# Optimization experiments

Measured on AMD Instinct MI355X. Metric: run time of the kernel, lower is better.

Reference implementation:

```python
import jax, jax.numpy as jnp
import numpy as np

B, S, E, H = 2, 2048, 1024, 16
DH = E // H


def setup_inputs() -> dict:
    key = jax.random.key(0)
    ks = jax.random.split(key, 9)
    s = 1.0 / np.sqrt(E)
    return {
        "queries": jax.random.normal(ks[0], (B, S, E), dtype=jnp.float32),
        "keys": jax.random.normal(ks[1], (B, S, E), dtype=jnp.float32),
        "values": jax.random.normal(ks[2], (B, S, E), dtype=jnp.float32),
        "mask": jax.random.randint(ks[3], (B, 1, 1, S), 0, 2, dtype=jnp.int32),
        "Wq": jax.random.normal(ks[4], (E, E), dtype=jnp.float32) * s,
        "Wk": jax.random.normal(ks[5], (E, E), dtype=jnp.float32) * s,
        "Wv": jax.random.normal(ks[6], (E, E), dtype=jnp.float32) * s,
        "Wo": jax.random.normal(ks[7], (E, E), dtype=jnp.float32) * s,
        "bo": jax.random.normal(ks[8], (E,), dtype=jnp.float32) * s,
    }


def reference(queries, keys, values, mask, Wq, Wk, Wv, Wo, bo):
    n, d_q, _ = queries.shape
    d_k = keys.shape[1]
    # Linear projections (torch Linear: x @ W.T), then split into heads
    q = (queries @ Wq.T).reshape(n, d_q, H, DH)
    k = (keys @ Wk.T).reshape(n, d_k, H, DH)
    v = (values @ Wv.T).reshape(n, d_k, H, DH)
    # [n, H, d_q, d_k] attention scores
    energy = jnp.einsum("nqhd,nkhd->nhqk", q, k)
    energy = jnp.where(mask == 0, jnp.float32(-1e20), energy)
    # NOTE: original scales by sqrt(key seq length), not head dim -- kept faithful
    attn = jax.nn.softmax(energy / jnp.sqrt(jnp.float32(d_k)), axis=3)
    out = jnp.einsum("nhql,nlhd->nqhd", attn, v).reshape(n, d_q, E)
    return out @ Wo.T + bo
```

## Files before the change

### kernel.cpp

```cpp
#include <hip/hip_runtime.h>
#include <hip/hip_bf16.h>

#define BB 2
#define SS 2048
#define EE 1024
#define HH 16
#define DHH 64

using bf16x8 = __attribute__((ext_vector_type(8))) __bf16;
using f32x4  = __attribute__((ext_vector_type(4))) float;

#if __has_builtin(__builtin_amdgcn_exp2f)
#define EXP2(x) __builtin_amdgcn_exp2f(x)
#else
#define EXP2(x) __exp2f(x)
#endif

static __device__ __forceinline__ unsigned short f2bf(float f) {
    unsigned int u = __float_as_uint(f);
    u += 0x7FFFu + ((u >> 16) & 1u);
    return (unsigned short)(u >> 16);
}

static __device__ __forceinline__ unsigned int pk2bf(float lo, float hi) {
    union { __hip_bfloat162 h2; unsigned int u; } c;
    c.h2 = __float22bfloat162_rn(float2{lo, hi});
    return c.u;
}

static __device__ __forceinline__ void async_load16(const void* g, void* l) {
    __builtin_amdgcn_global_load_lds(
        (const __attribute__((address_space(1))) unsigned int*)g,
        (__attribute__((address_space(3))) unsigned int*)l, 16, 0, 0);
}

__global__ void cvt_kernel(const float* __restrict__ W0, const float* __restrict__ W1,
                           const float* __restrict__ W2, const float* __restrict__ W3,
                           const float* __restrict__ X0, const float* __restrict__ X1,
                           const float* __restrict__ X2,
                           unsigned short* __restrict__ Wb,
                           unsigned short* __restrict__ D0, unsigned short* __restrict__ D1,
                           unsigned short* __restrict__ D2)
{
    const int z = blockIdx.y;
    const float* src;
    unsigned short* dst;
    if (z < 4) {
        if (blockIdx.x >= 512) return;
        src = (z == 0) ? W0 : (z == 1) ? W1 : (z == 2) ? W2 : W3;
        dst = Wb + (size_t)z * 1048576;
    } else {
        src = (z == 4) ? X0 : (z == 5) ? X1 : X2;
        dst = (z == 4) ? D0 : (z == 5) ? D1 : D2;
    }
    const size_t base = (size_t)blockIdx.x * 2048 + (size_t)threadIdx.x * 8;
    const float4 f0 = *(const float4*)(src + base);
    const float4 f1 = *(const float4*)(src + base + 4);
    uint4 p;
    p.x = pk2bf(f0.x, f0.y); p.y = pk2bf(f0.z, f0.w);
    p.z = pk2bf(f1.x, f1.y); p.w = pk2bf(f1.z, f1.w);
    *(uint4*)(dst + base) = p;
}

template<int MT, int NT, bool BF16OUT, bool VT_Z2>
__global__ __launch_bounds__(256, 3)
void gemm_xwt(const unsigned short* __restrict__ X0, const unsigned short* __restrict__ X1,
              const unsigned short* __restrict__ X2,
              const unsigned short* __restrict__ W0, const unsigned short* __restrict__ W1,
              const unsigned short* __restrict__ W2,
              void* __restrict__ Y0, void* __restrict__ Y1, void* __restrict__ Y2,
              const float* __restrict__ bias, int M, int N, int K,
              float s0, float s1, float s2)
{
    constexpr int BK = 32;
    constexpr int NI = MT / 32;
    constexpr int NJ = NT / 32;
    __shared__ __align__(16) unsigned short As[2][MT * BK];
    __shared__ __align__(16) unsigned short Bs[2][NT * BK];

    const int z = blockIdx.z;
    const unsigned short* __restrict__ X = (z == 0) ? X0 : ((z == 1) ? X1 : X2);
    const unsigned short* __restrict__ W = (z == 0) ? W0 : ((z == 1) ? W1 : W2);
    void* __restrict__ Y                 = (z == 0) ? Y0 : ((z == 1) ? Y1 : Y2);
    const float ysc                      = (z == 0) ? s0 : ((z == 1) ? s1 : s2);

    const int tid  = threadIdx.x;
    const int lane = tid & 63;
    const int wave = tid >> 6;
    const int wm   = (wave >> 1) * (MT / 2);
    const int wn   = (wave & 1) * (NT / 2);
    const int m0   = blockIdx.y * MT;
    const int n0   = blockIdx.x * NT;
    const int l16  = lane & 15;
    const int quad = lane >> 4;

    const int arow = lane >> 2;
    const int akc  = (lane & 3) * 8;

    f32x4 acc[NI][NJ];
    #pragma unroll
    for (int i = 0; i < NI; i++)
        #pragma unroll
        for (int j = 0; j < NJ; j++) acc[i][j] = f32x4{0.f, 0.f, 0.f, 0.f};

    auto stage = [&](int k0, int buf) {
        #pragma unroll
        for (int j = 0; j < NT / 64; j++) {
            const int rr = wave * (NT / 4) + j * 16;
            async_load16(W + (size_t)(n0 + rr + arow) * K + k0 + akc, Bs[buf] + rr * BK);
        }
        #pragma unroll
        for (int j = 0; j < MT / 64; j++) {
            const int rr = wave * (MT / 4) + j * 16;
            async_load16(X + (size_t)(m0 + rr + arow) * K + k0 + akc, As[buf] + rr * BK);
        }
    };

    stage(0, 0);
    const int niter = K / BK;
    for (int i = 0; i < niter; i++) {
        const int cur = i & 1;
        __syncthreads();
        if (i + 1 < niter) stage((i + 1) * BK, cur ^ 1);

        bf16x8 afrag[NI], bfrag[NJ];
        #pragma unroll
        for (int ii = 0; ii < NI; ii++)
            afrag[ii] = *(const bf16x8*)(As[cur] + (wm + ii * 16 + l16) * BK + quad * 8);
        #pragma unroll
        for (int j = 0; j < NJ; j++)
            bfrag[j] = *(const bf16x8*)(Bs[cur] + (wn + j * 16 + l16) * BK + quad * 8);
        #pragma unroll
        for (int ii = 0; ii < NI; ii++)
            #pragma unroll
            for (int j = 0; j < NJ; j++)
                acc[ii][j] = __builtin_amdgcn_mfma_f32_16x16x32_bf16(afrag[ii], bfrag[j], acc[ii][j], 0, 0, 0);
    }

    if (BF16OUT && VT_Z2 && z == 2) {
        #pragma unroll
        for (int i = 0; i < NI; i++) {
            const int row0 = m0 + wm + i * 16 + quad * 4;
            const int bb   = row0 >> 11;
            const int sx   = row0 & (SS - 1);
            #pragma unroll
            for (int j = 0; j < NJ; j++) {
                const int col = n0 + wn + j * 16 + l16;
                uint2 pck;
                pck.x = pk2bf(acc[i][j][0], acc[i][j][1]);
                pck.y = pk2bf(acc[i][j][2], acc[i][j][3]);
                *(uint2*)((unsigned short*)Y + (size_t)(bb * EE + col) * SS + sx) = pck;
            }
        }
    } else {
        #pragma unroll
        for (int i = 0; i < NI; i++) {
            #pragma unroll
            for (int j = 0; j < NJ; j++) {
                #pragma unroll
                for (int r = 0; r < 4; r++) {
                    const int row = m0 + wm + i * 16 + quad * 4 + r;
                    const int col = n0 + wn + j * 16 + l16;
                    const float v = acc[i][j][r];
                    if (BF16OUT) {
                        ((unsigned short*)Y)[(size_t)row * N + col] = f2bf(v * ysc);
                    } else {
                        ((float*)Y)[(size_t)row * N + col] = v + bias[col];
                    }
                }
            }
        }
    }
}

__global__ __launch_bounds__(256, 2)
void attn_kernel(const unsigned short* __restrict__ Qb,
                 const unsigned short* __restrict__ Kb,
                 const unsigned short* __restrict__ Vt,
                 const int* __restrict__ mask,
                 unsigned short* __restrict__ AO)
{
    constexpr int LDK = 68;
    constexpr int LDV = 68;
    constexpr int LDP = 68;
    __shared__ __align__(16) unsigned short Ks[64 * LDK];
    __shared__ __align__(16) unsigned short Vs[64 * LDV];
    __shared__ __align__(16) unsigned short Ps[4 * 32 * LDP];
    __shared__ __align__(16) float Msf[64];

    const int tid  = threadIdx.x;
    const int lane = tid & 63;
    const int wave = tid >> 6;
    const int l16  = lane & 15;
    const int quad = lane >> 4;

    const int linear = blockIdx.x;
    const int bh     = (linear & 7) * 4 + ((linear >> 3) & 3);
    const int qblk   = linear >> 5;
    const int b  = bh >> 4;
    const int h  = bh & 15;
    const int q0 = qblk * 128 + wave * 32;

    bf16x8 qf[2][2];
    #pragma unroll
    for (int g = 0; g < 2; g++) {
        const unsigned short* qptr = Qb + (size_t)(b * SS + q0 + g * 16 + l16) * EE + h * DHH;
        qf[g][0] = *(const bf16x8*)(qptr + quad * 8);
        qf[g][1] = *(const bf16x8*)(qptr + 32 + quad * 8);
    }

    float lsum[2] = {0.f, 0.f};
    f32x4 o_acc[2][4];
    #pragma unroll
    for (int g = 0; g < 2; g++)
        #pragma unroll
        for (int j = 0; j < 4; j++) o_acc[g][j] = f32x4{0.f, 0.f, 0.f, 0.f};

    unsigned short* Pw = Ps + wave * 32 * LDP;

    const int srow = tid >> 2;
    const int sc   = (tid & 3) * 16;

    uint4 kr0, kr1, vr0, vr1;
    int   mr = 0;
    auto gload = [&](int t0) {
        const unsigned short* kg = Kb + (size_t)(b * SS + t0 + srow) * EE + h * DHH + sc;
        kr0 = *(const uint4*)(kg);
        kr1 = *(const uint4*)(kg + 8);
        const unsigned short* vg = Vt + (size_t)(b * EE + h * DHH + srow) * SS + t0 + sc;
        vr0 = *(const uint4*)(vg);
        vr1 = *(const uint4*)(vg + 8);
        if (tid < 64) mr = mask[b * SS + t0 + tid];
    };
    gload(0);

    for (int t0 = 0; t0 < SS; t0 += 64) {
        __syncthreads();
        *(uint4*)(Ks + srow * LDK + sc)     = kr0;
        *(uint4*)(Ks + srow * LDK + sc + 8) = kr1;
        *(uint4*)(Vs + srow * LDV + sc)     = vr0;
        *(uint4*)(Vs + srow * LDV + sc + 8) = vr1;
        if (tid < 64) Msf[tid] = mr ? 0.0f : -150.0f;
        __syncthreads();

        if (t0 + 64 < SS) gload(t0 + 64);

        #pragma unroll
        for (int nt = 0; nt < 4; nt++) {
            bf16x8 kf0 = *(const bf16x8*)(Ks + (nt * 16 + l16) * LDK + quad * 8);
            bf16x8 kf1 = *(const bf16x8*)(Ks + (nt * 16 + l16) * LDK + 32 + quad * 8);
            const f32x4 cinit = *(const f32x4*)(Msf + nt * 16 + quad * 4);
            #pragma unroll
            for (int g = 0; g < 2; g++) {
                f32x4 a = __builtin_amdgcn_mfma_f32_16x16x32_bf16(kf0, qf[g][0], cinit, 0, 0, 0);
                a = __builtin_amdgcn_mfma_f32_16x16x32_bf16(kf1, qf[g][1], a, 0, 0, 0);
                const float p0 = EXP2(a[0]);
                const float p1 = EXP2(a[1]);
                const float p2 = EXP2(a[2]);
                const float p3 = EXP2(a[3]);
                lsum[g] += (p0 + p1) + (p2 + p3);
                uint2 pck;
                pck.x = pk2bf(p0, p1);
                pck.y = pk2bf(p2, p3);
                *(uint2*)(Pw + (g * 16 + l16) * LDP + nt * 16 + quad * 4) = pck;
            }
        }

        __builtin_amdgcn_s_waitcnt(0xC07F);

        #pragma unroll
        for (int s2 = 0; s2 < 2; s2++) {
            bf16x8 pf0 = *(const bf16x8*)(Pw + l16 * LDP + s2 * 32 + quad * 8);
            bf16x8 pf1 = *(const bf16x8*)(Pw + (16 + l16) * LDP + s2 * 32 + quad * 8);
            #pragma unroll
            for (int jg = 0; jg < 4; jg++) {
                bf16x8 vf = *(const bf16x8*)(Vs + (jg * 16 + l16) * LDV + s2 * 32 + quad * 8);
                o_acc[0][jg] = __builtin_amdgcn_mfma_f32_16x16x32_bf16(vf, pf0, o_acc[0][jg], 0, 0, 0);
                o_acc[1][jg] = __builtin_amdgcn_mfma_f32_16x16x32_bf16(vf, pf1, o_acc[1][jg], 0, 0, 0);
            }
        }
    }

    #pragma unroll
    for (int g = 0; g < 2; g++) {
        float ls = lsum[g];
        ls += __shfl_xor(ls, 16, 64);
        ls += __shfl_xor(ls, 32, 64);
        const float rl = 1.0f / ls;
        const size_t orow = (size_t)(b * SS + q0 + g * 16 + l16) * EE + h * DHH;
        #pragma unroll
        for (int jg = 0; jg < 4; jg++) {
            uint2 pck;
            pck.x = pk2bf(o_acc[g][jg][0] * rl, o_acc[g][jg][1] * rl);
            pck.y = pk2bf(o_acc[g][jg][2] * rl, o_acc[g][jg][3] * rl);
            *(uint2*)(AO + orow + jg * 16 + quad * 4) = pck;
        }
    }
}

extern "C" void kernel_launch(void* const* d_in, const int* in_sizes, int n_in,
                              void* d_out, int out_size, void* d_ws, size_t ws_size,
                              hipStream_t stream)
{
    (void)in_sizes; (void)n_in; (void)out_size; (void)ws_size;
    const float* queries = (const float*)d_in[0];
    const float* keys    = (const float*)d_in[1];
    const float* values  = (const float*)d_in[2];
    const int*   mask    = (const int*)d_in[3];
    const float* Wq      = (const float*)d_in[4];
    const float* Wk      = (const float*)d_in[5];
    const float* Wv      = (const float*)d_in[6];
    const float* Wo      = (const float*)d_in[7];
    const float* bo      = (const float*)d_in[8];

    const size_t NE = (size_t)BB * SS * EE;
    const size_t WE = (size_t)EE * EE;

    unsigned short* Xq  = (unsigned short*)d_out;
    unsigned short* Xk  = Xq + NE;
    unsigned short* Wb  = (unsigned short*)d_ws;
    unsigned short* Xv  = Wb + 4 * WE;
    unsigned short* Qb  = Xv + NE;
    unsigned short* Kb  = Qb + NE;
    unsigned short* Vtb = Kb + NE;
    unsigned short* AOb = Xv;

    const int M = BB * SS, N = EE, K = EE;
    const float qscale = 0.022097086912079608f * 1.4426950408889634f;

    cvt_kernel<<<dim3(2048, 7), 256, 0, stream>>>(
        Wq, Wk, Wv, Wo, queries, keys, values, Wb, Xq, Xk, Xv);

    dim3 gproj(N / 128, M / 128, 3);
    gemm_xwt<128, 128, true, true><<<gproj, 256, 0, stream>>>(
        Xq, Xk, Xv, Wb, Wb + WE, Wb + 2 * WE,
        (void*)Qb, (void*)Kb, (void*)Vtb, nullptr, M, N, K,
        qscale, 1.0f, 1.0f);

    attn_kernel<<<dim3(512), 256, 0, stream>>>(Qb, Kb, Vtb, mask, AOb);

    dim3 gout(N / 64, M / 64, 1);
    gemm_xwt<64, 64, false, false><<<gout, 256, 0, stream>>>(
        AOb, AOb, AOb, Wb + 3 * WE, Wb + 3 * WE, Wb + 3 * WE,
        d_out, d_out, d_out, bo, M, N, K, 1.0f, 1.0f, 1.0f);
}
```

Before: 243.2 us.

## Compact unmasked keys/values before attention and skip masked key tiles

Adds a compaction kernel that prefix-scans the key mask and gathers the kept K rows and V columns (V transposed through shared memory) into dense buffers. The attention kernel counts kept keys and loops only over ceil(nkeep/64) tiles, masking the tail of the last tile. The projection GEMM no longer writes V transposed. This roughly halves the attention work for a random mask, in exchange for an extra gather/transpose pass and a launch. Masked keys contribute exp(-1e20)≈0 in the reference, so skipping them is mathematically valid unless every key is masked.

```diff
diff --git a/kernel.cpp b/kernel.cpp
--- a/kernel.cpp
+++ b/kernel.cpp
@@ -62,7 +62,7 @@
     *(uint4*)(dst + base) = p;
 }
 
-template<int MT, int NT, bool BF16OUT, bool VT_Z2>
+template<int MT, int NT, bool BF16OUT>
 __global__ __launch_bounds__(256, 3)
 void gemm_xwt(const unsigned short* __restrict__ X0, const unsigned short* __restrict__ X1,
               const unsigned short* __restrict__ X2,
@@ -137,46 +137,120 @@
                 acc[ii][j] = __builtin_amdgcn_mfma_f32_16x16x32_bf16(afrag[ii], bfrag[j], acc[ii][j], 0, 0, 0);
     }
 
-    if (BF16OUT && VT_Z2 && z == 2) {
-        #pragma unroll
-        for (int i = 0; i < NI; i++) {
-            const int row0 = m0 + wm + i * 16 + quad * 4;
-            const int bb   = row0 >> 11;
-            const int sx   = row0 & (SS - 1);
-            #pragma unroll
-            for (int j = 0; j < NJ; j++) {
+    #pragma unroll
+    for (int i = 0; i < NI; i++) {
+        #pragma unroll
+        for (int j = 0; j < NJ; j++) {
+            #pragma unroll
+            for (int r = 0; r < 4; r++) {
+                const int row = m0 + wm + i * 16 + quad * 4 + r;
                 const int col = n0 + wn + j * 16 + l16;
-                uint2 pck;
-                pck.x = pk2bf(acc[i][j][0], acc[i][j][1]);
-                pck.y = pk2bf(acc[i][j][2], acc[i][j][3]);
-                *(uint2*)((unsigned short*)Y + (size_t)(bb * EE + col) * SS + sx) = pck;
-            }
-        }
-    } else {
-        #pragma unroll
-        for (int i = 0; i < NI; i++) {
-            #pragma unroll
-            for (int j = 0; j < NJ; j++) {
-                #pragma unroll
-                for (int r = 0; r < 4; r++) {
-                    const int row = m0 + wm + i * 16 + quad * 4 + r;
-                    const int col = n0 + wn + j * 16 + l16;
-                    const float v = acc[i][j][r];
-                    if (BF16OUT) {
-                        ((unsigned short*)Y)[(size_t)row * N + col] = f2bf(v * ysc);
-                    } else {
-                        ((float*)Y)[(size_t)row * N + col] = v + bias[col];
-                    }
+                const float v = acc[i][j][r];
+                if (BF16OUT) {
+                    ((unsigned short*)Y)[(size_t)row * N + col] = f2bf(v * ysc);
+                } else {
+                    ((float*)Y)[(size_t)row * N + col] = v + bias[col];
                 }
             }
         }
     }
 }
 
+__global__ __launch_bounds__(256, 1)
+void compact_kernel(const unsigned short* __restrict__ Kb,
+                    const unsigned short* __restrict__ Vb,
+                    const int* __restrict__ mask,
+                    unsigned short* __restrict__ Kc,
+                    unsigned short* __restrict__ Vtc)
+{
+    constexpr int LDE = 264;
+    __shared__ int srcIdx[64];
+    __shared__ int wsum[4];
+    __shared__ __align__(16) unsigned short T[64 * LDE];
+
+    const int tid  = threadIdx.x;
+    const int lane = tid & 63;
+    const int wave = tid >> 6;
+    const int b    = blockIdx.y;
+    const int t0   = blockIdx.x * 64;
+
+    const int base = tid * 8;
+    int v[8]; int run = 0;
+    #pragma unroll
+    for (int i = 0; i < 8; i++) { v[i] = (mask[b * SS + base + i] != 0) ? 1 : 0; run += v[i]; }
+
+    int inc = run;
+    #pragma unroll
+    for (int d = 1; d < 64; d <<= 1) {
+        int n = __shfl_up(inc, d, 64);
+        if (lane >= d) inc += n;
+    }
+    if (lane == 63) wsum[wave] = inc;
+    __syncthreads();
+    const int nkeep = wsum[0] + wsum[1] + wsum[2] + wsum[3];
+    if (t0 >= nkeep) return;
+
+    if (tid < 64) srcIdx[tid] = -1;
+    __syncthreads();
+
+    int r = inc - run;
+    #pragma unroll
+    for (int w = 0; w < 4; w++) if (w < wave) r += wsum[w];
+    #pragma unroll
+    for (int i = 0; i < 8; i++) {
+        if (v[i]) {
+            if (r >= t0 && r < t0 + 64) srcIdx[r - t0] = base + i;
+            r++;
+        }
+    }
+    __syncthreads();
+
+    {
+        const int j = tid >> 2, part = tid & 3;
+        const int s = srcIdx[j];
+        uint4* dst = (uint4*)(Kc + ((size_t)(b * SS + t0 + j)) * EE + part * 256);
+        if (s >= 0) {
+            const uint4* src = (const uint4*)(Kb + ((size_t)(b * SS + s)) * EE + part * 256);
+            #pragma unroll
+            for (int c = 0; c < 32; c++) dst[c] = src[c];
+        } else {
+            #pragma unroll
+            for (int c = 0; c < 32; c++) dst[c] = uint4{0, 0, 0, 0};
+        }
+    }
+
+    for (int ec = 0; ec < 4; ec++) {
+        __syncthreads();
+        {
+            const int j = tid >> 2, part = tid & 3;
+            const int s = srcIdx[j];
+            uint4* trow = (uint4*)(T + j * LDE + part * 64);
+            if (s >= 0) {
+                const uint4* src = (const uint4*)(Vb + ((size_t)(b * SS + s)) * EE + ec * 256 + part * 64);
+                #pragma unroll
+                for (int c = 0; c < 8; c++) trow[c] = src[c];
+            } else {
+                #pragma unroll
+                for (int c = 0; c < 8; c++) trow[c] = uint4{0, 0, 0, 0};
+            }
+        }
+        __syncthreads();
+        {
+            const int e = ec * 256 + tid;
+            unsigned short* drow = Vtc + ((size_t)(b * EE + e)) * SS + t0;
+            unsigned short tmp[64];
+            #pragma unroll
+            for (int j2 = 0; j2 < 64; j2++) tmp[j2] = T[j2 * LDE + tid];
+            #pragma unroll
+            for (int c = 0; c < 8; c++) ((uint4*)drow)[c] = ((const uint4*)tmp)[c];
+        }
+    }
+}
+
 __global__ __launch_bounds__(256, 2)
 void attn_kernel(const unsigned short* __restrict__ Qb,
-                 const unsigned short* __restrict__ Kb,
-                 const unsigned short* __restrict__ Vt,
+                 const unsigned short* __restrict__ Kc,
+                 const unsigned short* __restrict__ Vtc,
                  const int* __restrict__ mask,
                  unsigned short* __restrict__ AO)
 {
@@ -187,6 +261,7 @@
     __shared__ __align__(16) unsigned short Vs[64 * LDV];
     __shared__ __align__(16) unsigned short Ps[4 * 32 * LDP];
     __shared__ __align__(16) float Msf[64];
+    __shared__ int nk_s;
 
     const int tid  = threadIdx.x;
     const int lane = tid & 63;
@@ -201,6 +276,20 @@
     const int h  = bh & 15;
     const int q0 = qblk * 128 + wave * 32;
 
+    if (tid == 0) nk_s = 0;
+    __syncthreads();
+    {
+        int cnt = 0;
+        #pragma unroll
+        for (int i = 0; i < 8; i++) cnt += (mask[b * SS + tid * 8 + i] != 0) ? 1 : 0;
+        #pragma unroll
+        for (int d = 32; d >= 1; d >>= 1) cnt += __shfl_xor(cnt, d, 64);
+        if (lane == 0) atomicAdd(&nk_s, cnt);
+    }
+    __syncthreads();
+    const int nkeep  = nk_s;
+    const int ntiles = (nkeep + 63) >> 6;
+
     bf16x8 qf[2][2];
     #pragma unroll
     for (int g = 0; g < 2; g++) {
@@ -222,28 +311,27 @@
     const int sc   = (tid & 3) * 16;
 
     uint4 kr0, kr1, vr0, vr1;
-    int   mr = 0;
     auto gload = [&](int t0) {
-        const unsigned short* kg = Kb + (size_t)(b * SS + t0 + srow) * EE + h * DHH + sc;
+        const unsigned short* kg = Kc + (size_t)(b * SS + t0 + srow) * EE + h * DHH + sc;
         kr0 = *(const uint4*)(kg);
         kr1 = *(const uint4*)(kg + 8);
-        const unsigned short* vg = Vt + (size_t)(b * EE + h * DHH + srow) * SS + t0 + sc;
+        const unsigned short* vg = Vtc + (size_t)(b * EE + h * DHH + srow) * SS + t0 + sc;
         vr0 = *(const uint4*)(vg);
         vr1 = *(const uint4*)(vg + 8);
-        if (tid < 64) mr = mask[b * SS + t0 + tid];
     };
     gload(0);
 
-    for (int t0 = 0; t0 < SS; t0 += 64) {
+    for (int it = 0; it < ntiles; it++) {
+        const int t0 = it * 64;
         __syncthreads();
         *(uint4*)(Ks + srow * LDK + sc)     = kr0;
         *(uint4*)(Ks + srow * LDK + sc + 8) = kr1;
         *(uint4*)(Vs + srow * LDV + sc)     = vr0;
         *(uint4*)(Vs + srow * LDV + sc + 8) = vr1;
-        if (tid < 64) Msf[tid] = mr ? 0.0f : -150.0f;
+        if (tid < 64) Msf[tid] = (t0 + tid < nkeep) ? 0.0f : -150.0f;
         __syncthreads();
 
-        if (t0 + 64 < SS) gload(t0 + 64);
+        if (it + 1 < ntiles) gload(t0 + 64);
 
         #pragma unroll
         for (int nt = 0; nt < 4; nt++) {
@@ -318,11 +406,13 @@
 
     unsigned short* Xq  = (unsigned short*)d_out;
     unsigned short* Xk  = Xq + NE;
+    unsigned short* Kc  = (unsigned short*)d_out;
+    unsigned short* Vtc = Kc + NE;
     unsigned short* Wb  = (unsigned short*)d_ws;
     unsigned short* Xv  = Wb + 4 * WE;
     unsigned short* Qb  = Xv + NE;
     unsigned short* Kb  = Qb + NE;
-    unsigned short* Vtb = Kb + NE;
+    unsigned short* Vb  = Kb + NE;
     unsigned short* AOb = Xv;
 
     const int M = BB * SS, N = EE, K = EE;
@@ -332,15 +422,17 @@
         Wq, Wk, Wv, Wo, queries, keys, values, Wb, Xq, Xk, Xv);
 
     dim3 gproj(N / 128, M / 128, 3);
-    gemm_xwt<128, 128, true, true><<<gproj, 256, 0, stream>>>(
+    gemm_xwt<128, 128, true><<<gproj, 256, 0, stream>>>(
         Xq, Xk, Xv, Wb, Wb + WE, Wb + 2 * WE,
-        (void*)Qb, (void*)Kb, (void*)Vtb, nullptr, M, N, K,
+        (void*)Qb, (void*)Kb, (void*)Vb, nullptr, M, N, K,
         qscale, 1.0f, 1.0f);
 
-    attn_kernel<<<dim3(512), 256, 0, stream>>>(Qb, Kb, Vtb, mask, AOb);
+    compact_kernel<<<dim3(SS / 64, BB), 256, 0, stream>>>(Kb, Vb, mask, Kc, Vtc);
+
+    attn_kernel<<<dim3(512), 256, 0, stream>>>(Qb, Kc, Vtc, mask, AOb);
 
     dim3 gout(N / 64, M / 64, 1);
-    gemm_xwt<64, 64, false, false><<<gout, 256, 0, stream>>>(
+    gemm_xwt<64, 64, false><<<gout, 256, 0, stream>>>(
         AOb, AOb, AOb, Wb + 3 * WE, Wb + 3 * WE, Wb + 3 * WE,
         d_out, d_out, d_out, bo, M, N, K, 1.0f, 1.0f, 1.0f);
 }
```

Measured after the change: 236.4 us. 1.03x faster.
